# Performance work log

Measured on AMD Instinct MI355X. Metric: run time of the kernel, lower is better.

The kernel has to match this reference:

```python
import jax, jax.numpy as jnp
import numpy as np

# ---- config (matches init_kwargs) ----
C_IN, C_OUT = 128, 128
HYPER_OUT = 64            # hyper_out_size in DoubleConv
KB = C_IN // HYPER_OUT    # k = 2 blocks along input channels
HB = C_OUT // HYPER_OUT   # h = 2 blocks along output channels
Z_DIM, HID, SEIDEL_DIM = 128, 128, 48
R, F = 8, 3               # num_radii, filter size
BN_EPS = 1e-5


def _mlp_bank(z, W1, b1, W2, b2):
    # z: (S,); W1: (M,S,HID); returns (M, HID) embeddings from M distinct MLPs
    h = jax.nn.relu(jnp.einsum('s,msh->mh', z, W1) + b1)
    return jax.nn.relu(jnp.einsum('mh,mhg->mg', h, W2) + b2)


def _hyper(e, hw2, hb2, hw1, hb1):
    # Ha-style hypernetwork: e (Z_DIM,) -> kernel (64, 64, R, F, F)
    h_in = (e @ hw2 + hb2).reshape(HYPER_OUT, Z_DIM)
    h_fin = h_in @ hw1 + hb1  # (64, 64*R*F*F)
    return h_fin.reshape(HYPER_OUT, HYPER_OUT, R, F, F)


def _assemble(kernels, rows, cols):
    # kernels: (rows*cols, 64, 64, R, F, F) -> (rows*64, cols*64, R, F, F)
    k = kernels.reshape(rows, cols, HYPER_OUT, HYPER_OUT, R, F, F)
    k = k.transpose(0, 2, 1, 3, 4, 5, 6)
    return k.reshape(rows * HYPER_OUT, cols * HYPER_OUT, R, F, F)


def _interp_radii(w, Wdim):
    # trilinear interpolate (R,F,F)->(Wdim,F,F); F->F is identity, so linear along R
    # align_corners=False (PyTorch default)
    src = (jnp.arange(Wdim, dtype=jnp.float32) + 0.5) * (R / Wdim) - 0.5
    src = jnp.clip(src, 0.0, R - 1.0)
    i0 = jnp.floor(src).astype(jnp.int32)
    i1 = jnp.minimum(i0 + 1, R - 1)
    t = (src - i0.astype(jnp.float32))[None, None, :, None, None]
    return w[:, :, i0] * (1.0 - t) + w[:, :, i1] * t  # (co, ci, Wdim, F, F)


def _lri_conv(x, w):
    # x: (c_in, H, W); w: (c_out, c_in, R, F, F); padding=1, k=3
    c_in, H, W = x.shape
    xp = jnp.concatenate([x[:, -1:, :], x, x[:, :1, :]], axis=1)  # circular pad H
    xp = jnp.pad(xp, ((0, 0), (0, 0), (1, 1)))                    # zero pad W
    # patches laid out (c, di, dj) to match F.unfold
    pat = jnp.stack([xp[:, di:di + H, dj:dj + W]
                     for di in range(3) for dj in range(3)], axis=1)  # (c_in, 9, H, W)
    pat = pat.reshape(c_in * 9, H, W).transpose(1, 2, 0)              # (H, W, c_in*9)
    wi = _interp_radii(w, W)                                          # (co, ci, W, F, F)
    wu = wi.transpose(0, 2, 1, 3, 4).reshape(w.shape[0], W, c_in * 9) # (co, W, ci*9)
    return jnp.einsum('hwj,cwj->chw', pat, wu)                        # (co, H, W)


def _bn_eval(x, gamma, beta):
    # eval-mode BatchNorm2d with running_mean=0, running_var=1
    scale = gamma / jnp.sqrt(1.0 + BN_EPS)
    return x * scale[:, None, None] + beta[:, None, None]


def setup_inputs() -> dict:
    key = jax.random.key(0)
    ks = jax.random.split(key, 20)
    B, H, W = 2, 256, 128
    n1 = HB * KB   # 4 MLPs for first conv
    n2 = HB * HB   # 4 MLPs for second conv
    inp = {
        'x': jax.random.normal(ks[0], (B, C_IN, H, W), jnp.float32),
        'seidel': jax.random.normal(ks[1], (B, SEIDEL_DIM), jnp.float32),
        'm1_W1': jax.random.normal(ks[2], (n1, SEIDEL_DIM, HID)) * 0.1,
        'm1_b1': jnp.zeros((n1, HID)),
        'm1_W2': jax.random.normal(ks[3], (n1, HID, HID)) * 0.08,
        'm1_b2': jnp.zeros((n1, HID)),
        'm2_W1': jax.random.normal(ks[4], (n2, SEIDEL_DIM, HID)) * 0.1,
        'm2_b1': jnp.zeros((n2, HID)),
        'm2_W2': jax.random.normal(ks[5], (n2, HID, HID)) * 0.08,
        'm2_b2': jnp.zeros((n2, HID)),
        'hyp_w2': jax.random.normal(ks[6], (Z_DIM, HYPER_OUT * Z_DIM)) * 0.02,
        'hyp_b2': jnp.zeros((HYPER_OUT * Z_DIM,)),
        'hyp_w1': jax.random.normal(ks[7], (Z_DIM, HYPER_OUT * R * F * F)) * 0.02,
        'hyp_b1': jnp.zeros((HYPER_OUT * R * F * F,)),
        'bn1_g': jnp.ones((C_OUT,)), 'bn1_b': jnp.zeros((C_OUT,)),
        'bn2_g': jnp.ones((C_OUT,)), 'bn2_b': jnp.zeros((C_OUT,)),
    }
    return inp


def reference(x, seidel, m1_W1, m1_b1, m1_W2, m1_b2, m2_W1, m2_b1, m2_W2, m2_b2,
              hyp_w2, hyp_b2, hyp_w1, hyp_b1, bn1_g, bn1_b, bn2_g, bn2_b):
    hyper = lambda e: _hyper(e, hyp_w2, hyp_b2, hyp_w1, hyp_b1)

    def one_sample(x_i, z_i):
        emb1 = _mlp_bank(z_i, m1_W1, m1_b1, m1_W2, m1_b2)   # (h*k, Z)
        w1 = _assemble(jax.vmap(hyper)(emb1), HB, KB)        # (c_out, c_in, R, F, F)
        emb2 = _mlp_bank(z_i, m2_W1, m2_b1, m2_W2, m2_b2)   # (h*h, Z)
        w2 = _assemble(jax.vmap(hyper)(emb2), HB, HB)        # (c_out, c_out, R, F, F)
        y = jax.nn.relu(_bn_eval(_lri_conv(x_i, w1), bn1_g, bn1_b))
        y = jax.nn.relu(_bn_eval(_lri_conv(y, w2), bn2_g, bn2_b))
        return y

    return jax.vmap(one_sample)(x, seidel)  # (B, c_out, H, W)
```

## Files before the change

### kernel.cpp

```cpp
#include <hip/hip_runtime.h>
#include <hip/hip_bf16.h>

typedef _Float16 f16;
typedef _Float16 half8 __attribute__((ext_vector_type(8)));
typedef _Float16 half4_t __attribute__((ext_vector_type(4)));
typedef float floatx16 __attribute__((ext_vector_type(16)));

__device__ __forceinline__ void gll16(const void* g, void* l) {
    __builtin_amdgcn_global_load_lds(
        (const __attribute__((address_space(1))) void*)g,
        (__attribute__((address_space(3))) void*)l, 16, 0, 0);
}

__global__ __launch_bounds__(256) void embed_a(
    const float* __restrict__ seidel,
    const float* __restrict__ m1W1, const float* __restrict__ m1b1,
    const float* __restrict__ m1W2, const float* __restrict__ m1b2,
    const float* __restrict__ m2W1, const float* __restrict__ m2b1,
    const float* __restrict__ m2W2, const float* __restrict__ m2b2,
    float* __restrict__ eout)
{
    int combo = blockIdx.x;
    int s = combo >> 3, conv = (combo >> 2) & 1, m = combo & 3;
    const float* W1 = conv ? m2W1 : m1W1;
    const float* b1 = conv ? m2b1 : m1b1;
    const float* W2 = conv ? m2W2 : m1W2;
    const float* b2 = conv ? m2b2 : m1b2;
    __shared__ float zs[48], hbuf[128];
    int tid = threadIdx.x;
    if (tid < 48) zs[tid] = seidel[s*48 + tid];
    __syncthreads();
    if (tid < 128) {
        float a = b1[m*128 + tid];
        for (int i = 0; i < 48; ++i) a += zs[i] * W1[(m*48 + i)*128 + tid];
        hbuf[tid] = fmaxf(a, 0.f);
    }
    __syncthreads();
    if (tid < 128) {
        float a = b2[m*128 + tid];
        for (int i = 0; i < 128; ++i) a += hbuf[i] * W2[(m*128 + i)*128 + tid];
        eout[combo*128 + tid] = fmaxf(a, 0.f);
    }
}

__global__ __launch_bounds__(128) void embed_b3(
    const float* __restrict__ eout, const float* __restrict__ hw2,
    const float* __restrict__ hb2, float* __restrict__ hin)
{
    __shared__ float es[16][128];
    int tid = threadIdx.x;
    int j = blockIdx.x*128 + tid;
    for (int i = tid; i < 2048; i += 128) es[i >> 7][i & 127] = eout[i];
    __syncthreads();
    float acc[16];
    float b = hb2[j];
    #pragma unroll
    for (int c = 0; c < 16; ++c) acc[c] = b;
    for (int i = 0; i < 128; ++i) {
        float wv = hw2[(size_t)i*8192 + j];
        #pragma unroll
        for (int c = 0; c < 16; ++c) acc[c] += es[c][i]*wv;
    }
    #pragma unroll
    for (int c = 0; c < 16; ++c) hin[(size_t)c*8192 + j] = acc[c];
}

__global__ void hw1t_kernel(const float* __restrict__ in, float* __restrict__ out)
{
    __shared__ float tile[32][33];
    int j0 = blockIdx.x*32, k0 = blockIdx.y*32;
    int tx = threadIdx.x, ty = threadIdx.y;
    #pragma unroll
    for (int i = 0; i < 4; ++i) tile[ty + i*8][tx] = in[(size_t)(k0 + ty + i*8)*4608 + j0 + tx];
    __syncthreads();
    #pragma unroll
    for (int i = 0; i < 4; ++i) out[(size_t)(j0 + ty + i*8)*128 + k0 + tx] = tile[tx][ty + i*8];
}

__global__ __launch_bounds__(256) void hfin3_kernel(
    const float* __restrict__ hin, const float* __restrict__ hw1t,
    const float* __restrict__ hb1, f16* __restrict__ wtab)
{
    int c72 = blockIdx.x;
    int combo = blockIdx.y;
    int r = c72 / 9, tap = c72 - r*9;
    int s = combo >> 3, conv = (combo >> 2) & 1, m = combo & 3;
    __shared__ f16 A[64][136];
    __shared__ f16 B[64][136];
    __shared__ f16 ct[64][72];
    int tid = threadIdx.x;
    const float4* hsrc = (const float4*)(hin + (size_t)combo*8192);
    for (int i = tid; i < 2048; i += 256) {
        int a = i >> 5, k4 = (i & 31)*4;
        float4 v = hsrc[i];
        half4_t h; h[0]=(f16)v.x; h[1]=(f16)v.y; h[2]=(f16)v.z; h[3]=(f16)v.w;
        *(half4_t*)&A[a][k4] = h;
    }
    for (int i = tid; i < 2048; i += 256) {
        int b = i >> 5, k4 = (i & 31)*4;
        float4 v = *(const float4*)(hw1t + (size_t)(b*72 + c72)*128 + k4);
        half4_t h; h[0]=(f16)v.x; h[1]=(f16)v.y; h[2]=(f16)v.z; h[3]=(f16)v.w;
        *(half4_t*)&B[b][k4] = h;
    }
    __syncthreads();
    int lane = tid & 63, wid = tid >> 6;
    int wa = wid & 1, wb = wid >> 1;
    int l31 = lane & 31, lq = lane >> 5;
    floatx16 c = (floatx16)0.f;
    #pragma unroll
    for (int k = 0; k < 8; ++k) {
        half8 af = *(const half8*)&A[wa*32 + l31][k*16 + lq*8];
        half8 bf = *(const half8*)&B[wb*32 + l31][k*16 + lq*8];
        c = __builtin_amdgcn_mfma_f32_32x32x16_f16(af, bf, c, 0, 0, 0);
    }
    int bcol = wb*32 + l31;
    float bias = hb1[bcol*72 + c72];
    #pragma unroll
    for (int rr = 0; rr < 16; ++rr) {
        int a = wa*32 + (rr & 3) + 8*(rr >> 2) + 4*lq;
        ct[a][bcol] = (f16)(c[rr] + bias);
    }
    __syncthreads();
    {
        int a = tid & 63, q = tid >> 6;
        int chunk = (m & 1)*2 + (q >> 1);
        int co = (m >> 1)*64 + a;
        f16* dst = wtab + (((((size_t)(s*2 + conv)*8 + r)*4 + chunk)*9 + tap)*128 + co)*32
                   + (q & 1)*16;
        *(half8*)(dst)     = *(const half8*)&ct[a][q*16];
        *(half8*)(dst + 8) = *(const half8*)&ct[a][q*16 + 8];
    }
}

__global__ __launch_bounds__(256) void xpose_cast2(
    const float* __restrict__ in, f16* __restrict__ out, float4* __restrict__ zerop)
{
    __shared__ f16 tileT[128*136];
    int h = blockIdx.x, s = blockIdx.y;
    int tid = threadIdx.x;
    if (h == 0 && s == 0 && tid < 4) zerop[tid] = make_float4(0.f, 0.f, 0.f, 0.f);
    int cg = tid >> 5, q2 = tid & 31;
    const float* src = in + (size_t)s*4194304 + (size_t)h*128;
    for (int pass = 0; pass < 16; ++pass) {
        int c = pass*8 + cg;
        float4 v = *(const float4*)(src + (size_t)c*32768 + q2*4);
        tileT[(q2*4 + 0)*136 + c] = (f16)v.x;
        tileT[(q2*4 + 1)*136 + c] = (f16)v.y;
        tileT[(q2*4 + 2)*136 + c] = (f16)v.z;
        tileT[(q2*4 + 3)*136 + c] = (f16)v.w;
    }
    __syncthreads();
    int ww = tid >> 1, hf = tid & 1;
    const f16* srcT = &tileT[ww*136 + hf*64];
    f16* dst = out + (((size_t)(s*128 + ww)*256 + h)*128) + hf*64;
    #pragma unroll
    for (int i = 0; i < 8; ++i)
        *(float4*)(dst + i*8) = *(const float4*)(srcT + i*8);
}

__global__ void xpose_out(const float* __restrict__ in, float* __restrict__ out)
{
    __shared__ float tile[32][33];
    int sc = blockIdx.z;
    int w0 = blockIdx.x*32, h0 = blockIdx.y*32;
    int tx = threadIdx.x, ty = threadIdx.y;
    const float* src = in + ((size_t)sc*128 + w0)*256 + h0;
    #pragma unroll
    for (int i = 0; i < 4; ++i) tile[ty + i*8][tx] = src[(size_t)(ty + i*8)*256 + tx];
    __syncthreads();
    float* dst = out + ((size_t)sc*256 + h0)*128 + w0;
    #pragma unroll
    for (int i = 0; i < 4; ++i) dst[(size_t)(ty + i*8)*128 + tx] = tile[tx][ty + i*8];
}

template<int OUT_F16>
__global__ __launch_bounds__(512, 1) void conv_mfma12(
    const f16* __restrict__ xin,
    const f16* __restrict__ wtab,
    int conv,
    const float* __restrict__ bng, const float* __restrict__ bnb,
    void* __restrict__ outp,
    const float4* __restrict__ zerop)
{
    int b = blockIdx.x;
    int xcd = b & 7, i = b >> 3;
    int s = xcd >> 2;
    int w = (xcd & 3)*32 + i;
    const f16* xs  = xin  + (size_t)s*4194304;
    const f16* wts = wtab + (size_t)(s*2 + conv)*1179648;

    float fsrc = fminf(fmaxf((w + 0.5f)*0.0625f - 0.5f, 0.f), 7.f);
    int r0 = (int)fsrc, r1 = min(r0 + 1, 7);
    f16 th = (f16)(fsrc - (float)r0);

    __shared__ __align__(16) char sbuf[122880];

    int tid = threadIdx.x;
    int lane = tid & 63, wid = tid >> 6;
    int wc = wid & 1, wh = wid >> 1;
    int l31 = lane & 31, lq = lane >> 5;

    floatx16 acc[2][2];
    #pragma unroll
    for (int a = 0; a < 2; ++a)
        #pragma unroll
        for (int c = 0; c < 2; ++c) acc[a][c] = (floatx16)0.f;

    half8 wa[5], wb[5];

    auto loadw = [&](int hc) {
        int chunk = hc >> 1, half = hc & 1;
        #pragma unroll
        for (int p = 0; p < 5; ++p) {
            int sl = p*512 + tid;
            if (sl < 2304) {
                int tap = sl >> 8, rem = sl & 255;
                int part = rem >> 7, co = rem & 127;
                size_t off = (size_t)co*32 + half*16 + part*8;
                wa[p] = *(const half8*)(wts + (((size_t)(r0*4 + chunk)*9 + tap) << 12) + off);
                wb[p] = *(const half8*)(wts + (((size_t)(r1*4 + chunk)*9 + tap) << 12) + off);
            }
        }
    };
    auto stage_x = [&](int bsel, int hc) {
        char* xb = sbuf + 73728 + bsel*24576;
        #pragma unroll
        for (int it = 0; it < 3; ++it) {
            int id = it*512 + tid;
            int dj = id >> 9, part = (id >> 8) & 1, hp = id & 255;
            int wsg = w + dj - 1;
            const void* src = (wsg >= 0 && wsg < 128)
                ? (const void*)(xs + ((size_t)wsg*256 + hp)*128 + hc*16 + part*8)
                : (const void*)zerop;
            gll16(src, xb + (size_t)(it*512 + wid*64)*16);
        }
    };
    auto write_w = [&](int bsel) {
        char* wbase = sbuf + bsel*36864;
        #pragma unroll
        for (int p = 0; p < 5; ++p) {
            int sl = p*512 + tid;
            if (sl < 2304) {
                half8 o = wa[p] + (wb[p] - wa[p])*th;
                *(half8*)(wbase + (size_t)sl*16) = o;
            }
        }
    };

    loadw(0);
    stage_x(0, 0);
    write_w(0);
    __syncthreads();

    #pragma unroll 2
    for (int hc = 0; hc < 8; ++hc) {
        int cur = hc & 1;
        if (hc < 7) { loadw(hc + 1); stage_x(cur ^ 1, hc + 1); }
        __builtin_amdgcn_sched_barrier(0);
        const char* wbuf = sbuf + cur*36864;
        const f16* xb = (const f16*)(sbuf + 73728 + cur*24576);

        __builtin_amdgcn_s_setprio(1);
        #pragma unroll
        for (int tap = 0; tap < 4; ++tap) {
            int di = tap/3, dj = tap - di*3;
            half8 af0 = *(const half8*)(wbuf + (size_t)(tap*256 + lq*128 + wc*64 + l31)*16);
            half8 af1 = *(const half8*)(wbuf + (size_t)(tap*256 + lq*128 + wc*64 + 32 + l31)*16);
            int h0 = wh*64 + l31 + di - 1;
            half8 bf0 = *(const half8*)(xb + (size_t)(dj*512 + lq*256 + (h0 & 255))*8);
            half8 bf1 = *(const half8*)(xb + (size_t)(dj*512 + lq*256 + ((h0 + 32) & 255))*8);
            acc[0][0] = __builtin_amdgcn_mfma_f32_32x32x16_f16(af0, bf0, acc[0][0], 0, 0, 0);
            acc[0][1] = __builtin_amdgcn_mfma_f32_32x32x16_f16(af0, bf1, acc[0][1], 0, 0, 0);
            acc[1][0] = __builtin_amdgcn_mfma_f32_32x32x16_f16(af1, bf0, acc[1][0], 0, 0, 0);
            acc[1][1] = __builtin_amdgcn_mfma_f32_32x32x16_f16(af1, bf1, acc[1][1], 0, 0, 0);
        }
        __builtin_amdgcn_s_setprio(0);
        if (hc < 7) write_w(cur ^ 1);
        __builtin_amdgcn_s_setprio(1);
        #pragma unroll
        for (int tap = 4; tap < 9; ++tap) {
            int di = tap/3, dj = tap - di*3;
            half8 af0 = *(const half8*)(wbuf + (size_t)(tap*256 + lq*128 + wc*64 + l31)*16);
            half8 af1 = *(const half8*)(wbuf + (size_t)(tap*256 + lq*128 + wc*64 + 32 + l31)*16);
            int h0 = wh*64 + l31 + di - 1;
            half8 bf0 = *(const half8*)(xb + (size_t)(dj*512 + lq*256 + (h0 & 255))*8);
            half8 bf1 = *(const half8*)(xb + (size_t)(dj*512 + lq*256 + ((h0 + 32) & 255))*8);
            acc[0][0] = __builtin_amdgcn_mfma_f32_32x32x16_f16(af0, bf0, acc[0][0], 0, 0, 0);
            acc[0][1] = __builtin_amdgcn_mfma_f32_32x32x16_f16(af0, bf1, acc[0][1], 0, 0, 0);
            acc[1][0] = __builtin_amdgcn_mfma_f32_32x32x16_f16(af1, bf0, acc[1][0], 0, 0, 0);
            acc[1][1] = __builtin_amdgcn_mfma_f32_32x32x16_f16(af1, bf1, acc[1][1], 0, 0, 0);
        }
        __builtin_amdgcn_s_setprio(0);
        __syncthreads();
    }

    float rs = rsqrtf(1.f + 1e-5f);
    if (OUT_F16) {
        f16* otile = (f16*)sbuf;
        f16* yout = (f16*)outp + ((size_t)(s*128 + w)*256)*128;
        #pragma unroll
        for (int ph = 0; ph < 2; ++ph) {
            __syncthreads();
            if ((wh >> 1) == ph) {
                #pragma unroll
                for (int ct = 0; ct < 2; ++ct) {
                    #pragma unroll
                    for (int ht = 0; ht < 2; ++ht) {
                        int hrow = (wh & 1)*64 + ht*32 + l31;
                        #pragma unroll
                        for (int rq = 0; rq < 4; ++rq) {
                            int cb = wc*64 + ct*32 + rq*8 + lq*4;
                            float4 g4 = *(const float4*)&bng[cb];
                            float4 b4 = *(const float4*)&bnb[cb];
                            half4_t v;
                            #pragma unroll
                            for (int e = 0; e < 4; ++e) {
                                float g = (&g4.x)[e], bb = (&b4.x)[e];
                                v[e] = (f16)fmaxf(acc[ct][ht][rq*4 + e]*g*rs + bb, 0.f);
                            }
                            *(half4_t*)&otile[hrow*136 + cb] = v;
                        }
                    }
                }
            }
            __syncthreads();
            {
                int hrow = tid >> 2, qc = tid & 3;
                const f16* srcT = &otile[hrow*136 + qc*32];
                f16* d = yout + (size_t)(ph*128 + hrow)*128 + qc*32;
                #pragma unroll
                for (int k = 0; k < 4; ++k)
                    *(float4*)(d + k*8) = *(const float4*)(srcT + k*8);
            }
        }
    } else {
        #pragma unroll
        for (int ct = 0; ct < 2; ++ct) {
            #pragma unroll
            for (int ht = 0; ht < 2; ++ht) {
                int hrow = wh*64 + ht*32 + l31;
                #pragma unroll
                for (int r = 0; r < 16; ++r) {
                    int co = wc*64 + ct*32 + (r & 3) + 8*(r >> 2) + 4*lq;
                    float v = fmaxf(acc[ct][ht][r]*bng[co]*rs + bnb[co], 0.f);
                    ((float*)outp)[((size_t)(s*128 + co)*128 + w)*256 + hrow] = v;
                }
            }
        }
    }
}

extern "C" void kernel_launch(void* const* d_in, const int* in_sizes, int n_in,
                              void* d_out, int out_size, void* d_ws, size_t ws_size,
                              hipStream_t stream) {
    const float* x      = (const float*)d_in[0];
    const float* seidel = (const float*)d_in[1];
    const float* m1W1 = (const float*)d_in[2];
    const float* m1b1 = (const float*)d_in[3];
    const float* m1W2 = (const float*)d_in[4];
    const float* m1b2 = (const float*)d_in[5];
    const float* m2W1 = (const float*)d_in[6];
    const float* m2b1 = (const float*)d_in[7];
    const float* m2W2 = (const float*)d_in[8];
    const float* m2b2 = (const float*)d_in[9];
    const float* hw2  = (const float*)d_in[10];
    const float* hb2  = (const float*)d_in[11];
    const float* hw1  = (const float*)d_in[12];
    const float* hb1  = (const float*)d_in[13];
    const float* bn1g = (const float*)d_in[14];
    const float* bn1b = (const float*)d_in[15];
    const float* bn2g = (const float*)d_in[16];
    const float* bn2b = (const float*)d_in[17];
    float* outp = (float*)d_out;

    char* wsb = (char*)d_ws;
    f16*   wtab = (f16*)wsb;
    f16*   y1t  = (f16*)(wsb + 9437184);
    f16*   xt   = (f16*)(wsb + 26214400);
    float* y2t  = (float*)(wsb + 26214400);
    float4* zerop = (float4*)(wsb + 59768832);
    float* hin  = (float*)(wsb + 26214400);
    float* eout = (float*)(wsb + 26214400 + 524288);
    float* hw1t = (float*)(wsb + 26214400 + 1048576);

    embed_a<<<16, 256, 0, stream>>>(seidel, m1W1, m1b1, m1W2, m1b2,
                                    m2W1, m2b1, m2W2, m2b2, eout);
    embed_b3<<<64, 128, 0, stream>>>(eout, hw2, hb2, hin);
    hw1t_kernel<<<dim3(144, 4), dim3(32, 8), 0, stream>>>(hw1, hw1t);
    hfin3_kernel<<<dim3(72, 16), 256, 0, stream>>>(hin, hw1t, hb1, wtab);
    xpose_cast2<<<dim3(256, 2), 256, 0, stream>>>(x, xt, zerop);
    conv_mfma12<1><<<256, 512, 0, stream>>>(xt, wtab, 0, bn1g, bn1b, (void*)y1t, zerop);
    conv_mfma12<0><<<256, 512, 0, stream>>>(y1t, wtab, 1, bn2g, bn2b, (void*)y2t, zerop);
    xpose_out<<<dim3(4, 8, 256), dim3(32, 8), 0, stream>>>(y2t, outp);
}
```

Measured before the change: 147.0 us.

## Halve conv block to 4 waves with larger per-wave tiles; loop combos in hfin

The conv kernel now runs 256 threads (4 waves) per block instead of 8. Each wave computes 128 output rows times 64 channels with 8 accumulators, so each A-fragment load feeds four MFMAs instead of two. Weight and x staging loops are widened to match, the epilogue writes all 256 rows in one pass, and the unroll pragma and sched_barrier are removed. The hypernetwork final kernel now loops over the 16 combos inside 72 blocks so each block loads its B tile once, at the cost of far fewer blocks and serialized combos. The conv change adds register pressure and halves the waves available for latency hiding.

New measurement: 179.8 us. +22.3%, slower.

```diff
diff --git a/kernel.cpp b/kernel.cpp
--- a/kernel.cpp
+++ b/kernel.cpp
@@ -77,58 +77,61 @@
     for (int i = 0; i < 4; ++i) out[(size_t)(j0 + ty + i*8)*128 + k0 + tx] = tile[tx][ty + i*8];
 }
 
-__global__ __launch_bounds__(256) void hfin3_kernel(
+__global__ __launch_bounds__(256) void hfin4_kernel(
     const float* __restrict__ hin, const float* __restrict__ hw1t,
     const float* __restrict__ hb1, f16* __restrict__ wtab)
 {
     int c72 = blockIdx.x;
-    int combo = blockIdx.y;
     int r = c72 / 9, tap = c72 - r*9;
-    int s = combo >> 3, conv = (combo >> 2) & 1, m = combo & 3;
     __shared__ f16 A[64][136];
     __shared__ f16 B[64][136];
     __shared__ f16 ct[64][72];
     int tid = threadIdx.x;
-    const float4* hsrc = (const float4*)(hin + (size_t)combo*8192);
-    for (int i = tid; i < 2048; i += 256) {
-        int a = i >> 5, k4 = (i & 31)*4;
-        float4 v = hsrc[i];
-        half4_t h; h[0]=(f16)v.x; h[1]=(f16)v.y; h[2]=(f16)v.z; h[3]=(f16)v.w;
-        *(half4_t*)&A[a][k4] = h;
-    }
     for (int i = tid; i < 2048; i += 256) {
         int b = i >> 5, k4 = (i & 31)*4;
         float4 v = *(const float4*)(hw1t + (size_t)(b*72 + c72)*128 + k4);
         half4_t h; h[0]=(f16)v.x; h[1]=(f16)v.y; h[2]=(f16)v.z; h[3]=(f16)v.w;
         *(half4_t*)&B[b][k4] = h;
     }
-    __syncthreads();
     int lane = tid & 63, wid = tid >> 6;
-    int wa = wid & 1, wb = wid >> 1;
+    int wa_ = wid & 1, wb_ = wid >> 1;
     int l31 = lane & 31, lq = lane >> 5;
-    floatx16 c = (floatx16)0.f;
-    #pragma unroll
-    for (int k = 0; k < 8; ++k) {
-        half8 af = *(const half8*)&A[wa*32 + l31][k*16 + lq*8];
-        half8 bf = *(const half8*)&B[wb*32 + l31][k*16 + lq*8];
-        c = __builtin_amdgcn_mfma_f32_32x32x16_f16(af, bf, c, 0, 0, 0);
-    }
-    int bcol = wb*32 + l31;
+    int bcol = wb_*32 + l31;
     float bias = hb1[bcol*72 + c72];
-    #pragma unroll
-    for (int rr = 0; rr < 16; ++rr) {
-        int a = wa*32 + (rr & 3) + 8*(rr >> 2) + 4*lq;
-        ct[a][bcol] = (f16)(c[rr] + bias);
-    }
-    __syncthreads();
-    {
-        int a = tid & 63, q = tid >> 6;
-        int chunk = (m & 1)*2 + (q >> 1);
-        int co = (m >> 1)*64 + a;
-        f16* dst = wtab + (((((size_t)(s*2 + conv)*8 + r)*4 + chunk)*9 + tap)*128 + co)*32
-                   + (q & 1)*16;
-        *(half8*)(dst)     = *(const half8*)&ct[a][q*16];
-        *(half8*)(dst + 8) = *(const half8*)&ct[a][q*16 + 8];
+
+    for (int combo = 0; combo < 16; ++combo) {
+        const float4* hsrc = (const float4*)(hin + (size_t)combo*8192);
+        for (int i = tid; i < 2048; i += 256) {
+            int a = i >> 5, k4 = (i & 31)*4;
+            float4 v = hsrc[i];
+            half4_t h; h[0]=(f16)v.x; h[1]=(f16)v.y; h[2]=(f16)v.z; h[3]=(f16)v.w;
+            *(half4_t*)&A[a][k4] = h;
+        }
+        __syncthreads();
+        floatx16 c = (floatx16)0.f;
+        #pragma unroll
+        for (int k = 0; k < 8; ++k) {
+            half8 af = *(const half8*)&A[wa_*32 + l31][k*16 + lq*8];
+            half8 bf = *(const half8*)&B[bcol][k*16 + lq*8];
+            c = __builtin_amdgcn_mfma_f32_32x32x16_f16(af, bf, c, 0, 0, 0);
+        }
+        #pragma unroll
+        for (int rr = 0; rr < 16; ++rr) {
+            int a = wa_*32 + (rr & 3) + 8*(rr >> 2) + 4*lq;
+            ct[a][bcol] = (f16)(c[rr] + bias);
+        }
+        __syncthreads();
+        {
+            int s = combo >> 3, conv = (combo >> 2) & 1, m = combo & 3;
+            int a = tid & 63, q = tid >> 6;
+            int chunk = (m & 1)*2 + (q >> 1);
+            int co = (m >> 1)*64 + a;
+            f16* dst = wtab + (((((size_t)(s*2 + conv)*8 + r)*4 + chunk)*9 + tap)*128 + co)*32
+                       + (q & 1)*16;
+            *(half8*)(dst)     = *(const half8*)&ct[a][q*16];
+            *(half8*)(dst + 8) = *(const half8*)&ct[a][q*16 + 8];
+        }
+        __syncthreads();
     }
 }
 
@@ -174,7 +177,7 @@
 }
 
 template<int OUT_F16>
-__global__ __launch_bounds__(512, 1) void conv_mfma12(
+__global__ __launch_bounds__(256, 1) void conv_mfma13(
     const f16* __restrict__ xin,
     const f16* __restrict__ wtab,
     int conv,
@@ -197,53 +200,49 @@
 
     int tid = threadIdx.x;
     int lane = tid & 63, wid = tid >> 6;
-    int wc = wid & 1, wh = wid >> 1;
+    int wc = wid & 1, wh2 = wid >> 1;
     int l31 = lane & 31, lq = lane >> 5;
 
-    floatx16 acc[2][2];
+    floatx16 acc[2][4];
     #pragma unroll
     for (int a = 0; a < 2; ++a)
         #pragma unroll
-        for (int c = 0; c < 2; ++c) acc[a][c] = (floatx16)0.f;
-
-    half8 wa[5], wb[5];
+        for (int c = 0; c < 4; ++c) acc[a][c] = (floatx16)0.f;
+
+    half8 wa[9], wb[9];
 
     auto loadw = [&](int hc) {
         int chunk = hc >> 1, half = hc & 1;
         #pragma unroll
-        for (int p = 0; p < 5; ++p) {
-            int sl = p*512 + tid;
-            if (sl < 2304) {
-                int tap = sl >> 8, rem = sl & 255;
-                int part = rem >> 7, co = rem & 127;
-                size_t off = (size_t)co*32 + half*16 + part*8;
-                wa[p] = *(const half8*)(wts + (((size_t)(r0*4 + chunk)*9 + tap) << 12) + off);
-                wb[p] = *(const half8*)(wts + (((size_t)(r1*4 + chunk)*9 + tap) << 12) + off);
-            }
+        for (int p = 0; p < 9; ++p) {
+            int sl = p*256 + tid;
+            int tap = sl >> 8, rem = sl & 255;
+            int part = rem >> 7, co = rem & 127;
+            size_t off = (size_t)co*32 + half*16 + part*8;
+            wa[p] = *(const half8*)(wts + (((size_t)(r0*4 + chunk)*9 + tap) << 12) + off);
+            wb[p] = *(const half8*)(wts + (((size_t)(r1*4 + chunk)*9 + tap) << 12) + off);
         }
     };
     auto stage_x = [&](int bsel, int hc) {
         char* xb = sbuf + 73728 + bsel*24576;
         #pragma unroll
-        for (int it = 0; it < 3; ++it) {
-            int id = it*512 + tid;
+        for (int it = 0; it < 6; ++it) {
+            int id = it*256 + tid;
             int dj = id >> 9, part = (id >> 8) & 1, hp = id & 255;
             int wsg = w + dj - 1;
             const void* src = (wsg >= 0 && wsg < 128)
                 ? (const void*)(xs + ((size_t)wsg*256 + hp)*128 + hc*16 + part*8)
                 : (const void*)zerop;
-            gll16(src, xb + (size_t)(it*512 + wid*64)*16);
+            gll16(src, xb + (size_t)(it*256 + wid*64)*16);
         }
     };
     auto write_w = [&](int bsel) {
         char* wbase = sbuf + bsel*36864;
         #pragma unroll
-        for (int p = 0; p < 5; ++p) {
-            int sl = p*512 + tid;
-            if (sl < 2304) {
-                half8 o = wa[p] + (wb[p] - wa[p])*th;
-                *(half8*)(wbase + (size_t)sl*16) = o;
-            }
+        for (int p = 0; p < 9; ++p) {
+            int sl = p*256 + tid;
+            half8 o = wa[p] + (wb[p] - wa[p])*th;
+            *(half8*)(wbase + (size_t)sl*16) = o;
         }
     };
 
@@ -252,11 +251,9 @@
     write_w(0);
     __syncthreads();
 
-    #pragma unroll 2
     for (int hc = 0; hc < 8; ++hc) {
         int cur = hc & 1;
         if (hc < 7) { loadw(hc + 1); stage_x(cur ^ 1, hc + 1); }
-        __builtin_amdgcn_sched_barrier(0);
         const char* wbuf = sbuf + cur*36864;
         const f16* xb = (const f16*)(sbuf + 73728 + cur*24576);
 
@@ -266,13 +263,16 @@
             int di = tap/3, dj = tap - di*3;
             half8 af0 = *(const half8*)(wbuf + (size_t)(tap*256 + lq*128 + wc*64 + l31)*16);
             half8 af1 = *(const half8*)(wbuf + (size_t)(tap*256 + lq*128 + wc*64 + 32 + l31)*16);
-            int h0 = wh*64 + l31 + di - 1;
-            half8 bf0 = *(const half8*)(xb + (size_t)(dj*512 + lq*256 + (h0 & 255))*8);
-            half8 bf1 = *(const half8*)(xb + (size_t)(dj*512 + lq*256 + ((h0 + 32) & 255))*8);
-            acc[0][0] = __builtin_amdgcn_mfma_f32_32x32x16_f16(af0, bf0, acc[0][0], 0, 0, 0);
-            acc[0][1] = __builtin_amdgcn_mfma_f32_32x32x16_f16(af0, bf1, acc[0][1], 0, 0, 0);
-            acc[1][0] = __builtin_amdgcn_mfma_f32_32x32x16_f16(af1, bf0, acc[1][0], 0, 0, 0);
-            acc[1][1] = __builtin_amdgcn_mfma_f32_32x32x16_f16(af1, bf1, acc[1][1], 0, 0, 0);
+            int h0 = wh2*128 + l31 + di - 1;
+            half8 bf[4];
+            #pragma unroll
+            for (int ht = 0; ht < 4; ++ht)
+                bf[ht] = *(const half8*)(xb + (size_t)(dj*512 + lq*256 + ((h0 + ht*32) & 255))*8);
+            #pragma unroll
+            for (int ht = 0; ht < 4; ++ht) {
+                acc[0][ht] = __builtin_amdgcn_mfma_f32_32x32x16_f16(af0, bf[ht], acc[0][ht], 0, 0, 0);
+                acc[1][ht] = __builtin_amdgcn_mfma_f32_32x32x16_f16(af1, bf[ht], acc[1][ht], 0, 0, 0);
+            }
         }
         __builtin_amdgcn_s_setprio(0);
         if (hc < 7) write_w(cur ^ 1);
@@ -282,13 +282,16 @@
             int di = tap/3, dj = tap - di*3;
             half8 af0 = *(const half8*)(wbuf + (size_t)(tap*256 + lq*128 + wc*64 + l31)*16);
             half8 af1 = *(const half8*)(wbuf + (size_t)(tap*256 + lq*128 + wc*64 + 32 + l31)*16);
-            int h0 = wh*64 + l31 + di - 1;
-            half8 bf0 = *(const half8*)(xb + (size_t)(dj*512 + lq*256 + (h0 & 255))*8);
-            half8 bf1 = *(const half8*)(xb + (size_t)(dj*512 + lq*256 + ((h0 + 32) & 255))*8);
-            acc[0][0] = __builtin_amdgcn_mfma_f32_32x32x16_f16(af0, bf0, acc[0][0], 0, 0, 0);
-            acc[0][1] = __builtin_amdgcn_mfma_f32_32x32x16_f16(af0, bf1, acc[0][1], 0, 0, 0);
-            acc[1][0] = __builtin_amdgcn_mfma_f32_32x32x16_f16(af1, bf0, acc[1][0], 0, 0, 0);
-            acc[1][1] = __builtin_amdgcn_mfma_f32_32x32x16_f16(af1, bf1, acc[1][1], 0, 0, 0);
+            int h0 = wh2*128 + l31 + di - 1;
+            half8 bf[4];
+            #pragma unroll
+            for (int ht = 0; ht < 4; ++ht)
+                bf[ht] = *(const half8*)(xb + (size_t)(dj*512 + lq*256 + ((h0 + ht*32) & 255))*8);
+            #pragma unroll
+            for (int ht = 0; ht < 4; ++ht) {
+                acc[0][ht] = __builtin_amdgcn_mfma_f32_32x32x16_f16(af0, bf[ht], acc[0][ht], 0, 0, 0);
+                acc[1][ht] = __builtin_amdgcn_mfma_f32_32x32x16_f16(af1, bf[ht], acc[1][ht], 0, 0, 0);
+            }
         }
         __builtin_amdgcn_s_setprio(0);
         __syncthreads();
@@ -299,46 +302,38 @@
         f16* otile = (f16*)sbuf;
         f16* yout = (f16*)outp + ((size_t)(s*128 + w)*256)*128;
         #pragma unroll
-        for (int ph = 0; ph < 2; ++ph) {
-            __syncthreads();
-            if ((wh >> 1) == ph) {
+        for (int ct = 0; ct < 2; ++ct) {
+            #pragma unroll
+            for (int ht = 0; ht < 4; ++ht) {
+                int hrow = wh2*128 + ht*32 + l31;
                 #pragma unroll
-                for (int ct = 0; ct < 2; ++ct) {
+                for (int rq = 0; rq < 4; ++rq) {
+                    int cb = wc*64 + ct*32 + rq*8 + lq*4;
+                    float4 g4 = *(const float4*)&bng[cb];
+                    float4 b4 = *(const float4*)&bnb[cb];
+                    half4_t v;
                     #pragma unroll
-                    for (int ht = 0; ht < 2; ++ht) {
-                        int hrow = (wh & 1)*64 + ht*32 + l31;
-                        #pragma unroll
-                        for (int rq = 0; rq < 4; ++rq) {
-                            int cb = wc*64 + ct*32 + rq*8 + lq*4;
-                            float4 g4 = *(const float4*)&bng[cb];
-                            float4 b4 = *(const float4*)&bnb[cb];
-                            half4_t v;
-                            #pragma unroll
-                            for (int e = 0; e < 4; ++e) {
-                                float g = (&g4.x)[e], bb = (&b4.x)[e];
-                                v[e] = (f16)fmaxf(acc[ct][ht][rq*4 + e]*g*rs + bb, 0.f);
-                            }
-                            *(half4_t*)&otile[hrow*136 + cb] = v;
-                        }
+                    for (int e = 0; e < 4; ++e) {
+                        float g = (&g4.x)[e], bb = (&b4.x)[e];
+                        v[e] = (f16)fmaxf(acc[ct][ht][rq*4 + e]*g*rs + bb, 0.f);
                     }
+                    *(half4_t*)&otile[hrow*136 + cb] = v;
                 }
             }
-            __syncthreads();
-            {
-                int hrow = tid >> 2, qc = tid & 3;
-                const f16* srcT = &otile[hrow*136 + qc*32];
-                f16* d = yout + (size_t)(ph*128 + hrow)*128 + qc*32;
-                #pragma unroll
-                for (int k = 0; k < 4; ++k)
-                    *(float4*)(d + k*8) = *(const float4*)(srcT + k*8);
-            }
+        }
+        __syncthreads();
+        #pragma unroll
+        for (int k = 0; k < 16; ++k) {
+            int id = k*256 + tid;
+            int h = id >> 4, q = id & 15;
+            *(float4*)(yout + (size_t)h*128 + q*8) = *(const float4*)&otile[h*136 + q*8];
         }
     } else {
         #pragma unroll
         for (int ct = 0; ct < 2; ++ct) {
             #pragma unroll
-            for (int ht = 0; ht < 2; ++ht) {
-                int hrow = wh*64 + ht*32 + l31;
+            for (int ht = 0; ht < 4; ++ht) {
+                int hrow = wh2*128 + ht*32 + l31;
                 #pragma unroll
                 for (int r = 0; r < 16; ++r) {
                     int co = wc*64 + ct*32 + (r & 3) + 8*(r >> 2) + 4*lq;
@@ -387,9 +382,9 @@
                                     m2W1, m2b1, m2W2, m2b2, eout);
     embed_b3<<<64, 128, 0, stream>>>(eout, hw2, hb2, hin);
     hw1t_kernel<<<dim3(144, 4), dim3(32, 8), 0, stream>>>(hw1, hw1t);
-    hfin3_kernel<<<dim3(72, 16), 256, 0, stream>>>(hin, hw1t, hb1, wtab);
+    hfin4_kernel<<<72, 256, 0, stream>>>(hin, hw1t, hb1, wtab);
     xpose_cast2<<<dim3(256, 2), 256, 0, stream>>>(x, xt, zerop);
-    conv_mfma12<1><<<256, 512, 0, stream>>>(xt, wtab, 0, bn1g, bn1b, (void*)y1t, zerop);
-    conv_mfma12<0><<<256, 512, 0, stream>>>(y1t, wtab, 1, bn2g, bn2b, (void*)y2t, zerop);
+    conv_mfma13<1><<<256, 256, 0, stream>>>(xt, wtab, 0, bn1g, bn1b, (void*)y1t, zerop);
+    conv_mfma13<0><<<256, 256, 0, stream>>>(y1t, wtab, 1, bn2g, bn2b, (void*)y2t, zerop);
     xpose_out<<<dim3(4, 8, 256), dim3(32, 8), 0, stream>>>(y2t, outp);
 }
```
